# Performance work log

Measured on AMD Instinct MI355X. Metric: run time of the kernel, lower is better.

Reference implementation:

```python
import jax, jax.numpy as jnp
import numpy as np

K_CODES, D_DIM = 512, 64


def setup_inputs() -> dict:
    key = jax.random.key(0)
    k1, k2 = jax.random.split(key)
    x = jax.random.normal(k1, (32, D_DIM, 64, 64), dtype=jnp.float32)  # NCHW
    weight = jax.random.uniform(k2, (K_CODES, D_DIM), minval=-1.0 / K_CODES,
                                maxval=1.0 / K_CODES, dtype=jnp.float32)
    return {"x": x, "weight": weight}


def reference(x, weight):
    K = weight.shape[0]
    xp = jnp.transpose(x, (0, 2, 3, 1))          # [B, H, W, D]
    flat = xp.reshape(-1, weight.shape[1])       # [N, D]
    dist = (jnp.sum(flat * flat, axis=1, keepdims=True)
            + jnp.sum(weight * weight, axis=1)
            - 2.0 * flat @ weight.T)
    idx = jnp.argmin(dist, axis=1)               # [N]
    enc = jax.nn.one_hot(idx, K, dtype=jnp.float32)   # [N, K] one-hot scatter
    quantized = (enc @ weight).reshape(xp.shape)      # matmul codebook lookup
    commit_loss = jnp.mean(jnp.square(jax.lax.stop_gradient(quantized) - xp))
    vq_loss = jnp.mean(jnp.square(quantized - jax.lax.stop_gradient(xp)))
    loss = vq_loss + 1.0 * commit_loss           # commitment_cost = 1.0
    quant_st = xp + jax.lax.stop_gradient(quantized - xp)  # straight-through
    return (loss, jnp.transpose(quant_st, (0, 3, 1, 2)), enc, idx)
```

## Files before the change

### kernel.cpp

```cpp
#include <hip/hip_runtime.h>
#include <cfloat>

#define KC 512
#define DD 64
#define HW 4096
#define NPIX 131072
#define QSIZE 8388608
#define PXB 128
#define NBLK (NPIX / PXB)
#define NTH 512
#define MARGIN 4.0e-3f

typedef short short8 __attribute__((ext_vector_type(8)));
typedef float f32x4 __attribute__((ext_vector_type(4)));
typedef float nfloat4 __attribute__((ext_vector_type(4)));
typedef unsigned long long u64;

__device__ __forceinline__ unsigned short bf16_rne(float f) {
    unsigned int u = __float_as_uint(f);
    u += 0x7FFFu + ((u >> 16) & 1u);
    return (unsigned short)(u >> 16);
}

__global__ __launch_bounds__(1024) void prep(
    const float* __restrict__ w, float* __restrict__ w2g,
    uint4* __restrict__ wswz) {
  const int gt = blockIdx.x * 1024 + threadIdx.x;
  {
    int ct = gt >> 7, kc = (gt >> 6) & 1, ln = gt & 63;
    int n = ln & 15, q = ln >> 4;
    const float* wp = w + (ct * 16 + n) * DD + kc * 32 + q * 8;
    nfloat4 f0 = *(const nfloat4*)(wp);
    nfloat4 f1 = *(const nfloat4*)(wp + 4);
    uint4 u;
    u.x = (unsigned)bf16_rne(f0[0]) | ((unsigned)bf16_rne(f0[1]) << 16);
    u.y = (unsigned)bf16_rne(f0[2]) | ((unsigned)bf16_rne(f0[3]) << 16);
    u.z = (unsigned)bf16_rne(f1[0]) | ((unsigned)bf16_rne(f1[1]) << 16);
    u.w = (unsigned)bf16_rne(f1[2]) | ((unsigned)bf16_rne(f1[3]) << 16);
    wswz[gt] = u;
  }
  if (gt < KC) {
    const float* wk = w + gt * DD;
    float r0 = __fmul_rn(wk[0], wk[0]), r1 = __fmul_rn(wk[1], wk[1]),
          r2 = __fmul_rn(wk[2], wk[2]), r3 = __fmul_rn(wk[3], wk[3]),
          r4 = __fmul_rn(wk[4], wk[4]), r5 = __fmul_rn(wk[5], wk[5]),
          r6 = __fmul_rn(wk[6], wk[6]), r7 = __fmul_rn(wk[7], wk[7]);
    #pragma unroll
    for (int i = 8; i < DD; i += 8) {
      r0 = __fadd_rn(r0, __fmul_rn(wk[i+0], wk[i+0]));
      r1 = __fadd_rn(r1, __fmul_rn(wk[i+1], wk[i+1]));
      r2 = __fadd_rn(r2, __fmul_rn(wk[i+2], wk[i+2]));
      r3 = __fadd_rn(r3, __fmul_rn(wk[i+3], wk[i+3]));
      r4 = __fadd_rn(r4, __fmul_rn(wk[i+4], wk[i+4]));
      r5 = __fadd_rn(r5, __fmul_rn(wk[i+5], wk[i+5]));
      r6 = __fadd_rn(r6, __fmul_rn(wk[i+6], wk[i+6]));
      r7 = __fadd_rn(r7, __fmul_rn(wk[i+7], wk[i+7]));
    }
    w2g[gt] = __fadd_rn(__fadd_rn(__fadd_rn(r0, r1), __fadd_rn(r2, r3)),
                        __fadd_rn(__fadd_rn(r4, r5), __fadd_rn(r6, r7)));
  }
}

__global__ __launch_bounds__(NTH, 4) void vq_fused(
    const float* __restrict__ x, const float* __restrict__ w,
    const float* __restrict__ w2g, const uint4* __restrict__ wswz,
    float* __restrict__ out_q, float* __restrict__ out_enc,
    float* __restrict__ out_idx, double* __restrict__ partial) {

  __shared__ uint4 wlds[4096];
  __shared__ float w2s[KC];
  __shared__ u64 candm[PXB][8];
  __shared__ float Xs[PXB];
  __shared__ int sidx[PXB];
  __shared__ float sredf[8];

  const int tid = threadIdx.x;
  const int lane = tid & 63;
  const int wv = tid >> 6;
  const int bix = blockIdx.x;
  const int b = bix >> 5;
  const int p0 = (bix & 31) * PXB;
  const float* xt = x + (size_t)b * (DD * HW) + p0;

  #pragma unroll
  for (int s = 0; s < 8; ++s) wlds[tid + s * NTH] = wswz[tid + s * NTH];
  w2s[tid] = w2g[tid];
  if (tid < KC - NTH) w2s[tid + NTH] = w2g[tid + NTH];
  for (int i = tid; i < PXB * 8; i += NTH) ((u64*)candm)[i] = 0;

  if (tid < PXB) {
    const float* xp = xt + tid;
    float r0 = __fmul_rn(xp[0*HW], xp[0*HW]), r1 = __fmul_rn(xp[1*HW], xp[1*HW]),
          r2 = __fmul_rn(xp[2*HW], xp[2*HW]), r3 = __fmul_rn(xp[3*HW], xp[3*HW]),
          r4 = __fmul_rn(xp[4*HW], xp[4*HW]), r5 = __fmul_rn(xp[5*HW], xp[5*HW]),
          r6 = __fmul_rn(xp[6*HW], xp[6*HW]), r7 = __fmul_rn(xp[7*HW], xp[7*HW]);
    #pragma unroll
    for (int i = 8; i < DD; i += 8) {
      r0 = __fadd_rn(r0, __fmul_rn(xp[(size_t)(i+0)*HW], xp[(size_t)(i+0)*HW]));
      r1 = __fadd_rn(r1, __fmul_rn(xp[(size_t)(i+1)*HW], xp[(size_t)(i+1)*HW]));
      r2 = __fadd_rn(r2, __fmul_rn(xp[(size_t)(i+2)*HW], xp[(size_t)(i+2)*HW]));
      r3 = __fadd_rn(r3, __fmul_rn(xp[(size_t)(i+3)*HW], xp[(size_t)(i+3)*HW]));
      r4 = __fadd_rn(r4, __fmul_rn(xp[(size_t)(i+4)*HW], xp[(size_t)(i+4)*HW]));
      r5 = __fadd_rn(r5, __fmul_rn(xp[(size_t)(i+5)*HW], xp[(size_t)(i+5)*HW]));
      r6 = __fadd_rn(r6, __fmul_rn(xp[(size_t)(i+6)*HW], xp[(size_t)(i+6)*HW]));
      r7 = __fadd_rn(r7, __fmul_rn(xp[(size_t)(i+7)*HW], xp[(size_t)(i+7)*HW]));
    }
    Xs[tid] = __fadd_rn(__fadd_rn(__fadd_rn(r0, r1), __fadd_rn(r2, r3)),
                        __fadd_rn(__fadd_rn(r4, r5), __fadd_rn(r6, r7)));
  }

  const int am = lane & 15, aq = lane >> 4;
  const float* xa = xt + wv * 16 + am;
  short8 a0, a1;
  #pragma unroll
  for (int j = 0; j < 8; ++j) {
    a0[j] = (short)bf16_rne(-2.0f * xa[(size_t)(aq * 8 + j) * HW]);
    a1[j] = (short)bf16_rne(-2.0f * xa[(size_t)(32 + aq * 8 + j) * HW]);
  }

  __syncthreads();

  const short8* wl8 = (const short8*)wlds;
  const int cn = lane & 15;

  float m0 = FLT_MAX, m1 = FLT_MAX, m2 = FLT_MAX, m3 = FLT_MAX;
  for (int ct = 0; ct < 32; ++ct) {
    float wk2 = w2s[ct * 16 + cn];
    f32x4 acc = {wk2, wk2, wk2, wk2};
    acc = __builtin_amdgcn_mfma_f32_16x16x32_bf16(a0, wl8[ct * 128 + lane], acc, 0, 0, 0);
    acc = __builtin_amdgcn_mfma_f32_16x16x32_bf16(a1, wl8[ct * 128 + 64 + lane], acc, 0, 0, 0);
    m0 = fminf(m0, acc[0]); m1 = fminf(m1, acc[1]);
    m2 = fminf(m2, acc[2]); m3 = fminf(m3, acc[3]);
  }
  #pragma unroll
  for (int s = 1; s < 16; s <<= 1) {
    m0 = fminf(m0, __shfl_xor(m0, s));
    m1 = fminf(m1, __shfl_xor(m1, s));
    m2 = fminf(m2, __shfl_xor(m2, s));
    m3 = fminf(m3, __shfl_xor(m3, s));
  }
  const float t0 = m0 + MARGIN, t1 = m1 + MARGIN,
              t2 = m2 + MARGIN, t3 = m3 + MARGIN;

  for (int ct = 0; ct < 32; ++ct) {
    float wk2 = w2s[ct * 16 + cn];
    f32x4 acc = {wk2, wk2, wk2, wk2};
    acc = __builtin_amdgcn_mfma_f32_16x16x32_bf16(a0, wl8[ct * 128 + lane], acc, 0, 0, 0);
    acc = __builtin_amdgcn_mfma_f32_16x16x32_bf16(a1, wl8[ct * 128 + 64 + lane], acc, 0, 0, 0);
    u64 bm0 = __ballot(acc[0] <= t0);
    u64 bm1 = __ballot(acc[1] <= t1);
    u64 bm2 = __ballot(acc[2] <= t2);
    u64 bm3 = __ballot(acc[3] <= t3);
    if (lane < 4) {
      u64 mk = (lane == 0) ? bm0 : (lane == 1) ? bm1 : (lane == 2) ? bm2 : bm3;
      int word = ct >> 2, sh = (ct & 3) * 16;
      #pragma unroll
      for (int q = 0; q < 4; ++q) {
        u64 bits = (mk >> (q * 16)) & 0xFFFFull;
        if (bits) candm[wv * 16 + q * 4 + lane][word] |= bits << sh;
      }
    }
  }
  __syncthreads();

  {
    const int px = tid >> 2, part = tid & 3;
    const float X = Xs[px];
    const float* xr = xt + px;
    float bestd = FLT_MAX; int bk = 1 << 30;
    for (int wd = part * 2; wd < part * 2 + 2; ++wd) {
      u64 msk = candm[px][wd];
      while (msk) {
        int bit = __ffsll((unsigned long long)msk) - 1;
        msk &= msk - 1;
        int k = wd * 64 + bit;
        const float* wp = w + k * DD;
        float P = 0.f;
        #pragma unroll
        for (int dc = 0; dc < 16; ++dc) {
          nfloat4 w4 = *(const nfloat4*)(wp + dc * 4);
          P = __fmaf_rn(xr[(size_t)(dc * 4 + 0) * HW], w4[0], P);
          P = __fmaf_rn(xr[(size_t)(dc * 4 + 1) * HW], w4[1], P);
          P = __fmaf_rn(xr[(size_t)(dc * 4 + 2) * HW], w4[2], P);
          P = __fmaf_rn(xr[(size_t)(dc * 4 + 3) * HW], w4[3], P);
        }
        float dist = __fsub_rn(__fadd_rn(X, w2s[k]), __fadd_rn(P, P));
        if (dist < bestd || (dist == bestd && k < bk)) { bestd = dist; bk = k; }
      }
    }
    float od = __shfl_down(bestd, 1); int ok = __shfl_down(bk, 1);
    if ((lane & 3) < 3 && (od < bestd || (od == bestd && ok < bk))) { bestd = od; bk = ok; }
    od = __shfl_down(bestd, 2); ok = __shfl_down(bk, 2);
    if ((lane & 3) < 2 && (od < bestd || (od == bestd && ok < bk))) { bestd = od; bk = ok; }
    if (part == 0) {
      sidx[px] = bk;
      out_idx[bix * PXB + px] = (float)bk;
    }
  }
  __syncthreads();

  float lsum = 0.f;
  float* qb = out_q + (size_t)b * (DD * HW) + p0;
  for (int i = tid; i < PXB * DD; i += NTH) {
    int d = i >> 7, pp = i & 127;
    float qv = w[sidx[pp] * DD + d];
    float dv = qv - xt[(size_t)d * HW + pp];
    lsum = __fmaf_rn(dv, dv, lsum);
    __builtin_nontemporal_store(qv, qb + (size_t)d * HW + pp);
  }
  #pragma unroll
  for (int off = 32; off > 0; off >>= 1) lsum += __shfl_down(lsum, off);
  if (lane == 0) sredf[wv] = lsum;
  __syncthreads();
  if (tid == 0) {
    double t = 0.0;
    #pragma unroll
    for (int i = 0; i < 8; ++i) t += (double)sredf[i];
    partial[bix] = t;
  }

  float* basep = out_enc + (size_t)bix * (PXB * KC);
  for (int t = tid; t < 16383; t += NTH) {
    int u = 3 + 4 * t;
    nfloat4 v;
    #pragma unroll
    for (int j = 0; j < 4; ++j) {
      int e = u + j;
      v[j] = (sidx[e >> 9] == (e & 511)) ? 1.0f : 0.0f;
    }
    __builtin_nontemporal_store(v, (nfloat4*)(basep + u));
  }
  if (tid < 3) basep[tid] = (sidx[0] == tid) ? 1.0f : 0.0f;
  else if (tid == 3) basep[PXB * KC - 1] = (sidx[127] == 511) ? 1.0f : 0.0f;
}

__global__ void finish_kernel(const double* __restrict__ partial,
                              float* __restrict__ out) {
  int t = threadIdx.x;
  double s = partial[t] + partial[t + 256] + partial[t + 512] + partial[t + 768];
  #pragma unroll
  for (int off = 32; off > 0; off >>= 1) s += __shfl_down(s, off);
  __shared__ double sr[4];
  if ((t & 63) == 0) sr[t >> 6] = s;
  __syncthreads();
  if (t == 0)
    out[0] = (float)(2.0 * (sr[0] + sr[1] + sr[2] + sr[3]) / (double)QSIZE);
}

extern "C" void kernel_launch(void* const* d_in, const int* in_sizes, int n_in,
                              void* d_out, int out_size, void* d_ws, size_t ws_size,
                              hipStream_t stream) {
  const float* x = (const float*)d_in[0];
  const float* w = (const float*)d_in[1];
  float* out = (float*)d_out;
  float* out_q = out + 1;
  float* out_enc = out_q + QSIZE;
  float* out_idx = out_enc + (size_t)NPIX * KC;

  double* partial = (double*)d_ws;
  float* w2g = (float*)((char*)d_ws + 8192);
  uint4* wswz = (uint4*)((char*)d_ws + 16384);

  prep<<<4, 1024, 0, stream>>>(w, w2g, wswz);
  vq_fused<<<NBLK, NTH, 0, stream>>>(x, w, w2g, wswz, out_q, out_enc, out_idx, partial);
  finish_kernel<<<1, 256, 0, stream>>>(partial, out);
}
```

Before: 384.4 us.

## Split fused VQ kernel into argmin kernel and separate output-writing kernel

Splits the monolithic kernel into an argmin kernel that writes only indices and a lighter output kernel (64 pixels, 256 threads per block) that writes the quantized tensor, the one-hot encodings and the loss partials. The aim is to stop the large, LDS-heavy argmin blocks from also carrying the bandwidth-bound 268MB one-hot write, so the write phase can run at higher occupancy. In exchange it adds an extra launch, a global round-trip for the indices, and a second read of x.

```diff
diff --git a/kernel.cpp b/kernel.cpp
--- a/kernel.cpp
+++ b/kernel.cpp
@@ -10,6 +10,10 @@
 #define NBLK (NPIX / PXB)
 #define NTH 512
 #define MARGIN 4.0e-3f
+
+#define OPX 64
+#define ONB (NPIX / OPX)
+#define OTH 256
 
 typedef short short8 __attribute__((ext_vector_type(8)));
 typedef float f32x4 __attribute__((ext_vector_type(4)));
@@ -61,18 +65,15 @@
   }
 }
 
-__global__ __launch_bounds__(NTH, 4) void vq_fused(
+__global__ __launch_bounds__(NTH, 4) void vq_argmin(
     const float* __restrict__ x, const float* __restrict__ w,
     const float* __restrict__ w2g, const uint4* __restrict__ wswz,
-    float* __restrict__ out_q, float* __restrict__ out_enc,
-    float* __restrict__ out_idx, double* __restrict__ partial) {
+    float* __restrict__ out_idx) {
 
   __shared__ uint4 wlds[4096];
   __shared__ float w2s[KC];
   __shared__ u64 candm[PXB][8];
   __shared__ float Xs[PXB];
-  __shared__ int sidx[PXB];
-  __shared__ float sredf[8];
 
   const int tid = threadIdx.x;
   const int lane = tid & 63;
@@ -192,35 +193,40 @@
     if ((lane & 3) < 3 && (od < bestd || (od == bestd && ok < bk))) { bestd = od; bk = ok; }
     od = __shfl_down(bestd, 2); ok = __shfl_down(bk, 2);
     if ((lane & 3) < 2 && (od < bestd || (od == bestd && ok < bk))) { bestd = od; bk = ok; }
-    if (part == 0) {
-      sidx[px] = bk;
-      out_idx[bix * PXB + px] = (float)bk;
-    }
-  }
+    if (part == 0) out_idx[bix * PXB + px] = (float)bk;
+  }
+}
+
+__global__ __launch_bounds__(OTH, 4) void vq_out(
+    const float* __restrict__ x, const float* __restrict__ w,
+    const float* __restrict__ idx_f, float* __restrict__ out_q,
+    float* __restrict__ out_enc, double* __restrict__ partial) {
+
+  __shared__ int sidx[OPX];
+  __shared__ float sredf[4];
+
+  const int tid = threadIdx.x;
+  const int bix = blockIdx.x;
+  const int b = bix >> 6;
+  const int p0 = (bix & 63) * OPX;
+  const float* xt = x + (size_t)b * (DD * HW) + p0;
+
+  if (tid < OPX) sidx[tid] = (int)idx_f[bix * OPX + tid];
   __syncthreads();
 
   float lsum = 0.f;
   float* qb = out_q + (size_t)b * (DD * HW) + p0;
-  for (int i = tid; i < PXB * DD; i += NTH) {
-    int d = i >> 7, pp = i & 127;
+  for (int i = tid; i < OPX * DD; i += OTH) {
+    int d = i >> 6, pp = i & 63;
     float qv = w[sidx[pp] * DD + d];
     float dv = qv - xt[(size_t)d * HW + pp];
     lsum = __fmaf_rn(dv, dv, lsum);
     __builtin_nontemporal_store(qv, qb + (size_t)d * HW + pp);
   }
-  #pragma unroll
-  for (int off = 32; off > 0; off >>= 1) lsum += __shfl_down(lsum, off);
-  if (lane == 0) sredf[wv] = lsum;
-  __syncthreads();
-  if (tid == 0) {
-    double t = 0.0;
-    #pragma unroll
-    for (int i = 0; i < 8; ++i) t += (double)sredf[i];
-    partial[bix] = t;
-  }
-
-  float* basep = out_enc + (size_t)bix * (PXB * KC);
-  for (int t = tid; t < 16383; t += NTH) {
+
+  float* basep = out_enc + (size_t)bix * (OPX * KC);
+  nfloat4* zb4 = (nfloat4*)(basep + 3);
+  for (int t = tid; t < (OPX * KC - 4) / 4; t += OTH) {
     int u = 3 + 4 * t;
     nfloat4 v;
     #pragma unroll
@@ -228,16 +234,29 @@
       int e = u + j;
       v[j] = (sidx[e >> 9] == (e & 511)) ? 1.0f : 0.0f;
     }
-    __builtin_nontemporal_store(v, (nfloat4*)(basep + u));
+    __builtin_nontemporal_store(v, zb4 + t);
   }
   if (tid < 3) basep[tid] = (sidx[0] == tid) ? 1.0f : 0.0f;
-  else if (tid == 3) basep[PXB * KC - 1] = (sidx[127] == 511) ? 1.0f : 0.0f;
+  else if (tid == 3) basep[OPX * KC - 1] = (sidx[OPX - 1] == 511) ? 1.0f : 0.0f;
+
+  #pragma unroll
+  for (int off = 32; off > 0; off >>= 1) lsum += __shfl_down(lsum, off);
+  if ((tid & 63) == 0) sredf[tid >> 6] = lsum;
+  __syncthreads();
+  if (tid == 0) {
+    double t = 0.0;
+    #pragma unroll
+    for (int i = 0; i < 4; ++i) t += (double)sredf[i];
+    partial[bix] = t;
+  }
 }
 
 __global__ void finish_kernel(const double* __restrict__ partial,
                               float* __restrict__ out) {
   int t = threadIdx.x;
-  double s = partial[t] + partial[t + 256] + partial[t + 512] + partial[t + 768];
+  double s = 0.0;
+  #pragma unroll
+  for (int i = 0; i < 8; ++i) s += partial[t + 256 * i];
   #pragma unroll
   for (int off = 32; off > 0; off >>= 1) s += __shfl_down(s, off);
   __shared__ double sr[4];
@@ -258,10 +277,11 @@
   float* out_idx = out_enc + (size_t)NPIX * KC;
 
   double* partial = (double*)d_ws;
-  float* w2g = (float*)((char*)d_ws + 8192);
-  uint4* wswz = (uint4*)((char*)d_ws + 16384);
+  float* w2g = (float*)((char*)d_ws + 16384);
+  uint4* wswz = (uint4*)((char*)d_ws + 24576);
 
   prep<<<4, 1024, 0, stream>>>(w, w2g, wswz);
-  vq_fused<<<NBLK, NTH, 0, stream>>>(x, w, w2g, wswz, out_q, out_enc, out_idx, partial);
+  vq_argmin<<<NBLK, NTH, 0, stream>>>(x, w, w2g, wswz, out_idx);
+  vq_out<<<ONB, OTH, 0, stream>>>(x, w, out_idx, out_q, out_enc, partial);
   finish_kernel<<<1, 256, 0, stream>>>(partial, out);
 }
```

Result: slower. 418.6 us (+8.9%).

## Read swizzled codebook from global/L2 instead of LDS, halve block size

Applied to the files above, without the earlier changes.

Removes the 64KB LDS staging of the swizzled bf16 codebook and has each wave load its B fragments straight from global memory (L2-resident) inside the MFMA loops, which are unrolled by two. Blocks shrink to 64 pixels and 256 threads, doubling the grid, and the occupancy hint rises to 6. The intent is to drop the per-block LDS fill and the LDS capacity limit on residency, at the cost of repeated L2 traffic for the codebook in both distance passes. Workspace offsets and the final reduction are adjusted for the larger partial array.

```diff
diff --git a/kernel.cpp b/kernel.cpp
--- a/kernel.cpp
+++ b/kernel.cpp
@@ -6,9 +6,9 @@
 #define HW 4096
 #define NPIX 131072
 #define QSIZE 8388608
-#define PXB 128
+#define PXB 64
 #define NBLK (NPIX / PXB)
-#define NTH 512
+#define NTH 256
 #define MARGIN 4.0e-3f
 
 typedef short short8 __attribute__((ext_vector_type(8)));
@@ -61,32 +61,30 @@
   }
 }
 
-__global__ __launch_bounds__(NTH, 4) void vq_fused(
+__global__ __launch_bounds__(NTH, 6) void vq_fused(
     const float* __restrict__ x, const float* __restrict__ w,
-    const float* __restrict__ w2g, const uint4* __restrict__ wswz,
+    const float* __restrict__ w2g, const short8* __restrict__ wsw8,
     float* __restrict__ out_q, float* __restrict__ out_enc,
     float* __restrict__ out_idx, double* __restrict__ partial) {
 
-  __shared__ uint4 wlds[4096];
   __shared__ float w2s[KC];
   __shared__ u64 candm[PXB][8];
   __shared__ float Xs[PXB];
   __shared__ int sidx[PXB];
-  __shared__ float sredf[8];
+  __shared__ float sredf[4];
 
   const int tid = threadIdx.x;
   const int lane = tid & 63;
   const int wv = tid >> 6;
   const int bix = blockIdx.x;
-  const int b = bix >> 5;
-  const int p0 = (bix & 31) * PXB;
+  const int b = bix >> 6;
+  const int p0 = (bix & 63) * PXB;
   const float* xt = x + (size_t)b * (DD * HW) + p0;
 
-  #pragma unroll
-  for (int s = 0; s < 8; ++s) wlds[tid + s * NTH] = wswz[tid + s * NTH];
   w2s[tid] = w2g[tid];
-  if (tid < KC - NTH) w2s[tid + NTH] = w2g[tid + NTH];
-  for (int i = tid; i < PXB * 8; i += NTH) ((u64*)candm)[i] = 0;
+  w2s[tid + NTH] = w2g[tid + NTH];
+  ((u64*)candm)[tid] = 0;
+  ((u64*)candm)[tid + NTH] = 0;
 
   if (tid < PXB) {
     const float* xp = xt + tid;
@@ -120,15 +118,17 @@
 
   __syncthreads();
 
-  const short8* wl8 = (const short8*)wlds;
   const int cn = lane & 15;
 
   float m0 = FLT_MAX, m1 = FLT_MAX, m2 = FLT_MAX, m3 = FLT_MAX;
+  #pragma unroll 2
   for (int ct = 0; ct < 32; ++ct) {
     float wk2 = w2s[ct * 16 + cn];
+    short8 b0 = wsw8[ct * 128 + lane];
+    short8 b1 = wsw8[ct * 128 + 64 + lane];
     f32x4 acc = {wk2, wk2, wk2, wk2};
-    acc = __builtin_amdgcn_mfma_f32_16x16x32_bf16(a0, wl8[ct * 128 + lane], acc, 0, 0, 0);
-    acc = __builtin_amdgcn_mfma_f32_16x16x32_bf16(a1, wl8[ct * 128 + 64 + lane], acc, 0, 0, 0);
+    acc = __builtin_amdgcn_mfma_f32_16x16x32_bf16(a0, b0, acc, 0, 0, 0);
+    acc = __builtin_amdgcn_mfma_f32_16x16x32_bf16(a1, b1, acc, 0, 0, 0);
     m0 = fminf(m0, acc[0]); m1 = fminf(m1, acc[1]);
     m2 = fminf(m2, acc[2]); m3 = fminf(m3, acc[3]);
   }
@@ -142,11 +142,14 @@
   const float t0 = m0 + MARGIN, t1 = m1 + MARGIN,
               t2 = m2 + MARGIN, t3 = m3 + MARGIN;
 
+  #pragma unroll 2
   for (int ct = 0; ct < 32; ++ct) {
     float wk2 = w2s[ct * 16 + cn];
+    short8 b0 = wsw8[ct * 128 + lane];
+    short8 b1 = wsw8[ct * 128 + 64 + lane];
     f32x4 acc = {wk2, wk2, wk2, wk2};
-    acc = __builtin_amdgcn_mfma_f32_16x16x32_bf16(a0, wl8[ct * 128 + lane], acc, 0, 0, 0);
-    acc = __builtin_amdgcn_mfma_f32_16x16x32_bf16(a1, wl8[ct * 128 + 64 + lane], acc, 0, 0, 0);
+    acc = __builtin_amdgcn_mfma_f32_16x16x32_bf16(a0, b0, acc, 0, 0, 0);
+    acc = __builtin_amdgcn_mfma_f32_16x16x32_bf16(a1, b1, acc, 0, 0, 0);
     u64 bm0 = __ballot(acc[0] <= t0);
     u64 bm1 = __ballot(acc[1] <= t1);
     u64 bm2 = __ballot(acc[2] <= t2);
@@ -202,7 +205,7 @@
   float lsum = 0.f;
   float* qb = out_q + (size_t)b * (DD * HW) + p0;
   for (int i = tid; i < PXB * DD; i += NTH) {
-    int d = i >> 7, pp = i & 127;
+    int d = i >> 6, pp = i & 63;
     float qv = w[sidx[pp] * DD + d];
     float dv = qv - xt[(size_t)d * HW + pp];
     lsum = __fmaf_rn(dv, dv, lsum);
@@ -215,12 +218,12 @@
   if (tid == 0) {
     double t = 0.0;
     #pragma unroll
-    for (int i = 0; i < 8; ++i) t += (double)sredf[i];
+    for (int i = 0; i < 4; ++i) t += (double)sredf[i];
     partial[bix] = t;
   }
 
   float* basep = out_enc + (size_t)bix * (PXB * KC);
-  for (int t = tid; t < 16383; t += NTH) {
+  for (int t = tid; t < (PXB * KC - 4) / 4; t += NTH) {
     int u = 3 + 4 * t;
     nfloat4 v;
     #pragma unroll
@@ -231,13 +234,15 @@
     __builtin_nontemporal_store(v, (nfloat4*)(basep + u));
   }
   if (tid < 3) basep[tid] = (sidx[0] == tid) ? 1.0f : 0.0f;
-  else if (tid == 3) basep[PXB * KC - 1] = (sidx[127] == 511) ? 1.0f : 0.0f;
+  else if (tid == 3) basep[PXB * KC - 1] = (sidx[PXB - 1] == 511) ? 1.0f : 0.0f;
 }
 
 __global__ void finish_kernel(const double* __restrict__ partial,
                               float* __restrict__ out) {
   int t = threadIdx.x;
-  double s = partial[t] + partial[t + 256] + partial[t + 512] + partial[t + 768];
+  double s = 0.0;
+  #pragma unroll
+  for (int i = 0; i < 8; ++i) s += partial[t + 256 * i];
   #pragma unroll
   for (int off = 32; off > 0; off >>= 1) s += __shfl_down(s, off);
   __shared__ double sr[4];
@@ -258,10 +263,11 @@
   float* out_idx = out_enc + (size_t)NPIX * KC;
 
   double* partial = (double*)d_ws;
-  float* w2g = (float*)((char*)d_ws + 8192);
-  uint4* wswz = (uint4*)((char*)d_ws + 16384);
+  float* w2g = (float*)((char*)d_ws + 16384);
+  uint4* wswz = (uint4*)((char*)d_ws + 24576);
 
   prep<<<4, 1024, 0, stream>>>(w, w2g, wswz);
-  vq_fused<<<NBLK, NTH, 0, stream>>>(x, w, w2g, wswz, out_q, out_enc, out_idx, partial);
+  vq_fused<<<NBLK, NTH, 0, stream>>>(x, w, w2g, (const short8*)wswz,
+                                     out_q, out_enc, out_idx, partial);
   finish_kernel<<<1, 256, 0, stream>>>(partial, out);
 }
```

New measurement: 423.4 us. 10.1% more time.

## Process two pixel tiles per block and overlap next-tile prelude with stores

Applied to the files above, without the earlier changes.

Each block now handles two 128-pixel tiles, which halves the grid and amortizes the codebook and norm LDS loads over both tiles. The second tile's x loads and norm computation are issued alongside the first tile's quantized and one-hot output stores, so reads can overlap writes. Block-wide syncs are replaced by barriers that wait only on LDS counters, letting outstanding global stores drain past the barrier. The cost is fewer, longer blocks, which risks lower parallelism and tail imbalance, plus closer reasoning about LDS reuse hazards between tiles.

```diff
diff --git a/kernel.cpp b/kernel.cpp
--- a/kernel.cpp
+++ b/kernel.cpp
@@ -7,7 +7,8 @@
 #define NPIX 131072
 #define QSIZE 8388608
 #define PXB 128
-#define NBLK (NPIX / PXB)
+#define NTILE (NPIX / PXB)
+#define NBLK (NTILE / 2)
 #define NTH 512
 #define MARGIN 4.0e-3f
 
@@ -20,6 +21,12 @@
     unsigned int u = __float_as_uint(f);
     u += 0x7FFFu + ((u >> 16) & 1u);
     return (unsigned short)(u >> 16);
+}
+
+__device__ __forceinline__ void barrier_lds_only() {
+    asm volatile("s_waitcnt lgkmcnt(0)" ::: "memory");
+    __builtin_amdgcn_s_barrier();
+    __builtin_amdgcn_sched_barrier(0);
 }
 
 __global__ __launch_bounds__(1024) void prep(
@@ -61,33 +68,12 @@
   }
 }
 
-__global__ __launch_bounds__(NTH, 4) void vq_fused(
-    const float* __restrict__ x, const float* __restrict__ w,
-    const float* __restrict__ w2g, const uint4* __restrict__ wswz,
-    float* __restrict__ out_q, float* __restrict__ out_enc,
-    float* __restrict__ out_idx, double* __restrict__ partial) {
-
-  __shared__ uint4 wlds[4096];
-  __shared__ float w2s[KC];
-  __shared__ u64 candm[PXB][8];
-  __shared__ float Xs[PXB];
-  __shared__ int sidx[PXB];
-  __shared__ float sredf[8];
-
-  const int tid = threadIdx.x;
-  const int lane = tid & 63;
-  const int wv = tid >> 6;
-  const int bix = blockIdx.x;
-  const int b = bix >> 5;
-  const int p0 = (bix & 31) * PXB;
-  const float* xt = x + (size_t)b * (DD * HW) + p0;
-
-  #pragma unroll
-  for (int s = 0; s < 8; ++s) wlds[tid + s * NTH] = wswz[tid + s * NTH];
-  w2s[tid] = w2g[tid];
-  if (tid < KC - NTH) w2s[tid + NTH] = w2g[tid + NTH];
-  for (int i = tid; i < PXB * 8; i += NTH) ((u64*)candm)[i] = 0;
-
+
+__device__ __forceinline__ void tile_prelude(
+    const float* __restrict__ xt, float* Xs, u64 (*candm)[8],
+    short8& a0, short8& a1, int tid, int lane, int wv) {
+  ((u64*)candm)[tid] = 0;
+  ((u64*)candm)[tid + NTH] = 0;
   if (tid < PXB) {
     const float* xp = xt + tid;
     float r0 = __fmul_rn(xp[0*HW], xp[0*HW]), r1 = __fmul_rn(xp[1*HW], xp[1*HW]),
@@ -108,21 +94,19 @@
     Xs[tid] = __fadd_rn(__fadd_rn(__fadd_rn(r0, r1), __fadd_rn(r2, r3)),
                         __fadd_rn(__fadd_rn(r4, r5), __fadd_rn(r6, r7)));
   }
-
   const int am = lane & 15, aq = lane >> 4;
   const float* xa = xt + wv * 16 + am;
-  short8 a0, a1;
   #pragma unroll
   for (int j = 0; j < 8; ++j) {
     a0[j] = (short)bf16_rne(-2.0f * xa[(size_t)(aq * 8 + j) * HW]);
     a1[j] = (short)bf16_rne(-2.0f * xa[(size_t)(32 + aq * 8 + j) * HW]);
   }
-
-  __syncthreads();
-
-  const short8* wl8 = (const short8*)wlds;
+}
+
+__device__ __forceinline__ void tile_screen(
+    const short8* wl8, const float* w2s, u64 (*candm)[8],
+    short8 a0, short8 a1, int lane, int wv) {
   const int cn = lane & 15;
-
   float m0 = FLT_MAX, m1 = FLT_MAX, m2 = FLT_MAX, m3 = FLT_MAX;
   for (int ct = 0; ct < 32; ++ct) {
     float wk2 = w2s[ct * 16 + cn];
@@ -141,7 +125,6 @@
   }
   const float t0 = m0 + MARGIN, t1 = m1 + MARGIN,
               t2 = m2 + MARGIN, t3 = m3 + MARGIN;
-
   for (int ct = 0; ct < 32; ++ct) {
     float wk2 = w2s[ct * 16 + cn];
     f32x4 acc = {wk2, wk2, wk2, wk2};
@@ -161,46 +144,50 @@
       }
     }
   }
-  __syncthreads();
-
-  {
-    const int px = tid >> 2, part = tid & 3;
-    const float X = Xs[px];
-    const float* xr = xt + px;
-    float bestd = FLT_MAX; int bk = 1 << 30;
-    for (int wd = part * 2; wd < part * 2 + 2; ++wd) {
-      u64 msk = candm[px][wd];
-      while (msk) {
-        int bit = __ffsll((unsigned long long)msk) - 1;
-        msk &= msk - 1;
-        int k = wd * 64 + bit;
-        const float* wp = w + k * DD;
-        float P = 0.f;
-        #pragma unroll
-        for (int dc = 0; dc < 16; ++dc) {
-          nfloat4 w4 = *(const nfloat4*)(wp + dc * 4);
-          P = __fmaf_rn(xr[(size_t)(dc * 4 + 0) * HW], w4[0], P);
-          P = __fmaf_rn(xr[(size_t)(dc * 4 + 1) * HW], w4[1], P);
-          P = __fmaf_rn(xr[(size_t)(dc * 4 + 2) * HW], w4[2], P);
-          P = __fmaf_rn(xr[(size_t)(dc * 4 + 3) * HW], w4[3], P);
-        }
-        float dist = __fsub_rn(__fadd_rn(X, w2s[k]), __fadd_rn(P, P));
-        if (dist < bestd || (dist == bestd && k < bk)) { bestd = dist; bk = k; }
+}
+
+__device__ __forceinline__ void tile_refine(
+    const float* __restrict__ xt, const float* __restrict__ w,
+    const float* w2s, const float* Xs, const u64 (*candm)[8],
+    int* sidx, float* __restrict__ out_idx, int bix, int tid, int lane) {
+  const int px = tid >> 2, part = tid & 3;
+  const float X = Xs[px];
+  const float* xr = xt + px;
+  float bestd = FLT_MAX; int bk = 1 << 30;
+  for (int wd = part * 2; wd < part * 2 + 2; ++wd) {
+    u64 msk = candm[px][wd];
+    while (msk) {
+      int bit = __ffsll((unsigned long long)msk) - 1;
+      msk &= msk - 1;
+      int k = wd * 64 + bit;
+      const float* wp = w + k * DD;
+      float P = 0.f;
+      #pragma unroll
+      for (int dc = 0; dc < 16; ++dc) {
+        nfloat4 w4 = *(const nfloat4*)(wp + dc * 4);
+        P = __fmaf_rn(xr[(size_t)(dc * 4 + 0) * HW], w4[0], P);
+        P = __fmaf_rn(xr[(size_t)(dc * 4 + 1) * HW], w4[1], P);
+        P = __fmaf_rn(xr[(size_t)(dc * 4 + 2) * HW], w4[2], P);
+        P = __fmaf_rn(xr[(size_t)(dc * 4 + 3) * HW], w4[3], P);
       }
-    }
-    float od = __shfl_down(bestd, 1); int ok = __shfl_down(bk, 1);
-    if ((lane & 3) < 3 && (od < bestd || (od == bestd && ok < bk))) { bestd = od; bk = ok; }
-    od = __shfl_down(bestd, 2); ok = __shfl_down(bk, 2);
-    if ((lane & 3) < 2 && (od < bestd || (od == bestd && ok < bk))) { bestd = od; bk = ok; }
-    if (part == 0) {
-      sidx[px] = bk;
-      out_idx[bix * PXB + px] = (float)bk;
-    }
-  }
-  __syncthreads();
-
+      float dist = __fsub_rn(__fadd_rn(X, w2s[k]), __fadd_rn(P, P));
+      if (dist < bestd || (dist == bestd && k < bk)) { bestd = dist; bk = k; }
+    }
+  }
+  float od = __shfl_down(bestd, 1); int ok = __shfl_down(bk, 1);
+  if ((lane & 3) < 3 && (od < bestd || (od == bestd && ok < bk))) { bestd = od; bk = ok; }
+  od = __shfl_down(bestd, 2); ok = __shfl_down(bk, 2);
+  if ((lane & 3) < 2 && (od < bestd || (od == bestd && ok < bk))) { bestd = od; bk = ok; }
+  if (part == 0) {
+    sidx[px] = bk;
+    out_idx[bix * PXB + px] = (float)bk;
+  }
+}
+
+__device__ __forceinline__ float tile_quant(
+    const float* __restrict__ xt, const float* __restrict__ w,
+    const int* sidx, float* __restrict__ qb, int tid) {
   float lsum = 0.f;
-  float* qb = out_q + (size_t)b * (DD * HW) + p0;
   for (int i = tid; i < PXB * DD; i += NTH) {
     int d = i >> 7, pp = i & 127;
     float qv = w[sidx[pp] * DD + d];
@@ -208,18 +195,11 @@
     lsum = __fmaf_rn(dv, dv, lsum);
     __builtin_nontemporal_store(qv, qb + (size_t)d * HW + pp);
   }
-  #pragma unroll
-  for (int off = 32; off > 0; off >>= 1) lsum += __shfl_down(lsum, off);
-  if (lane == 0) sredf[wv] = lsum;
-  __syncthreads();
-  if (tid == 0) {
-    double t = 0.0;
-    #pragma unroll
-    for (int i = 0; i < 8; ++i) t += (double)sredf[i];
-    partial[bix] = t;
-  }
-
-  float* basep = out_enc + (size_t)bix * (PXB * KC);
+  return lsum;
+}
+
+__device__ __forceinline__ void tile_enc(
+    const int* sidx, float* __restrict__ basep, int tid) {
   for (int t = tid; t < 16383; t += NTH) {
     int u = 3 + 4 * t;
     nfloat4 v;
@@ -232,6 +212,83 @@
   }
   if (tid < 3) basep[tid] = (sidx[0] == tid) ? 1.0f : 0.0f;
   else if (tid == 3) basep[PXB * KC - 1] = (sidx[127] == 511) ? 1.0f : 0.0f;
+}
+
+__global__ __launch_bounds__(NTH, 4) void vq_fused(
+    const float* __restrict__ x, const float* __restrict__ w,
+    const float* __restrict__ w2g, const uint4* __restrict__ wswz,
+    float* __restrict__ out_q, float* __restrict__ out_enc,
+    float* __restrict__ out_idx, double* __restrict__ partial) {
+
+  __shared__ uint4 wlds[4096];
+  __shared__ float w2s[KC];
+  __shared__ u64 candm[PXB][8];
+  __shared__ float Xs[PXB];
+  __shared__ int sidx[PXB];
+  __shared__ float sredf[8];
+
+  const int tid = threadIdx.x;
+  const int lane = tid & 63;
+  const int wv = tid >> 6;
+
+  const int bix0 = blockIdx.x;
+  const int b0 = bix0 >> 5;
+  const int q0 = (bix0 & 31) * PXB;
+  const float* xt0 = x + (size_t)b0 * (DD * HW) + q0;
+  const int bix1 = blockIdx.x + NBLK;
+  const int b1 = bix1 >> 5;
+  const int q1 = (bix1 & 31) * PXB;
+  const float* xt1 = x + (size_t)b1 * (DD * HW) + q1;
+
+  #pragma unroll
+  for (int s = 0; s < 8; ++s) wlds[tid + s * NTH] = wswz[tid + s * NTH];
+  w2s[tid] = w2g[tid];
+
+  short8 a0, a1;
+  tile_prelude(xt0, Xs, candm, a0, a1, tid, lane, wv);
+  __syncthreads();
+
+  const short8* wl8 = (const short8*)wlds;
+
+  tile_screen(wl8, w2s, candm, a0, a1, lane, wv);
+  barrier_lds_only();
+  tile_refine(xt0, w, w2s, Xs, candm, sidx, out_idx, bix0, tid, lane);
+  barrier_lds_only();
+
+  tile_prelude(xt1, Xs, candm, a0, a1, tid, lane, wv);
+  {
+    float lsum = tile_quant(xt0, w, sidx, out_q + (size_t)b0 * (DD * HW) + q0, tid);
+    #pragma unroll
+    for (int off = 32; off > 0; off >>= 1) lsum += __shfl_down(lsum, off);
+    if (lane == 0) sredf[wv] = lsum;
+  }
+  tile_enc(sidx, out_enc + (size_t)bix0 * (PXB * KC), tid);
+  barrier_lds_only();
+  if (tid == 0) {
+    double t = 0.0;
+    #pragma unroll
+    for (int i = 0; i < 8; ++i) t += (double)sredf[i];
+    partial[bix0] = t;
+  }
+
+  tile_screen(wl8, w2s, candm, a0, a1, lane, wv);
+  barrier_lds_only();
+  tile_refine(xt1, w, w2s, Xs, candm, sidx, out_idx, bix1, tid, lane);
+  barrier_lds_only();
+  {
+    float lsum = tile_quant(xt1, w, sidx, out_q + (size_t)b1 * (DD * HW) + q1, tid);
+    #pragma unroll
+    for (int off = 32; off > 0; off >>= 1) lsum += __shfl_down(lsum, off);
+    if (lane == 0) sredf[wv] = lsum;
+  }
+  tile_enc(sidx, out_enc + (size_t)bix1 * (PXB * KC), tid);
+  barrier_lds_only();
+  if (tid == 0) {
+    double t = 0.0;
+    #pragma unroll
+    for (int i = 0; i < 8; ++i) t += (double)sredf[i];
+    partial[bix1] = t;
+  }
 }
 
 __global__ void finish_kernel(const double* __restrict__ partial,
```

New measurement: 381.2 us. About the same (-0.8%).
